# Optimization experiments

Measured on AMD Instinct MI355X. Metric: run time of the kernel, lower is better.

## Reference

```python
import jax, jax.numpy as jnp
import numpy as np

NUM_CLASSES = 26
IGNORE_LABEL = 0
LAMBDA_SMOOTH = 1.0
EPSILON = 1e-05
# static indices of valid (non-ignored) classes
_VALID = np.array([c for c in range(NUM_CLASSES) if c != IGNORE_LABEL])


def setup_inputs() -> dict:
    key = jax.random.key(0)
    k1, k2, k3 = jax.random.split(key, 3)
    B, D, H, W = 1, 160, 192, 224
    fixed_label_map = jax.random.randint(k1, (B, D, H, W), 0, NUM_CLASSES, dtype=jnp.int32)
    warped_moving_label_map = jax.random.randint(k2, (B, D, H, W), 0, NUM_CLASSES, dtype=jnp.int32)
    vector_field = jax.random.normal(k3, (B, 3, D, H, W), dtype=jnp.float32)
    return {
        'fixed_label_map': fixed_label_map,
        'warped_moving_label_map': warped_moving_label_map,
        'vector_field': vector_field,
    }


def _soft_dice(fixed, moving):
    # Equivalent to one-hot expansion + sum over (B,D,H,W), but computed
    # directly from integer labels via histogram counts (single pass).
    f = fixed.reshape(-1)
    m = moving.reshape(-1)
    fixed_vol = jnp.bincount(f, length=NUM_CLASSES).astype(jnp.float32)
    moving_vol = jnp.bincount(m, length=NUM_CLASSES).astype(jnp.float32)
    # intersection[c] = #{voxels: f==c and m==c}
    inter = jnp.bincount(f, weights=(f == m).astype(jnp.float32), length=NUM_CLASSES)
    dice = (2.0 * inter + EPSILON) / (fixed_vol + moving_vol + EPSILON)
    return 1.0 - dice[_VALID].mean()


def _diffusion(vf):
    # vf: [B, 3, D, H, W]
    dz = vf[:, :, 1:, :, :] - vf[:, :, :-1, :, :]
    dy = vf[:, :, :, 1:, :] - vf[:, :, :, :-1, :]
    dx = vf[:, :, :, :, 1:] - vf[:, :, :, :, :-1]
    return (jnp.mean(dz * dz) + jnp.mean(dy * dy) + jnp.mean(dx * dx)) / 3.0


def reference(fixed_label_map, warped_moving_label_map, vector_field):
    similarity_loss = _soft_dice(fixed_label_map, warped_moving_label_map)
    smoothness_loss = _diffusion(vector_field)
    total_loss = similarity_loss + LAMBDA_SMOOTH * smoothness_loss
    return (total_loss, similarity_loss, smoothness_loss)
```

## Files before the change

kernel.cpp:

```cpp
#include <hip/hip_runtime.h>


namespace {
constexpr int NC    = 26;
constexpr int Dd    = 160, Hh = 192, Ww = 224;
constexpr int W4    = Ww / 4;
constexpr int PL4   = Hh * W4;
constexpr int N4L   = Dd * Hh * Ww / 4;
constexpr int JSTRIDE = 33;
constexpr int NBINS   = NC * JSTRIDE;
constexpr int TPB     = 1024;
constexpr int WPB     = TPB / 64;
constexpr int HIST_BLOCKS = 210;
constexpr int HT          = HIST_BLOCKS * TPB;
constexpr int SLAB    = 6;
constexpr int DCH     = 5;
constexpr int DIFF_WAVES  = 3 * (Dd / DCH) * (Hh / SLAB);
constexpr int DIFF_BLOCKS = DIFF_WAVES / WPB;
constexpr int FUSED_BLOCKS = DIFF_BLOCKS + HIST_BLOCKS;
constexpr int GRP         = 8;
constexpr int DIFF_GRPS   = DIFF_BLOCKS / GRP;
constexpr int PAIRED_GRPS = 2 * DIFF_GRPS;
}

__global__ void init_ws_kernel(unsigned int* __restrict__ joint,
                               double* __restrict__ sums) {
    int i = blockIdx.x * blockDim.x + threadIdx.x;
    if (i < NBINS) joint[i] = 0u;
    if (i < 3)     sums[i]  = 0.0;
}

__device__ __forceinline__ void hist_path(
        int hb,
        const int4* __restrict__ f4,
        const int4* __restrict__ m4,
        unsigned int* __restrict__ gj) {
    __shared__ unsigned int h[NBINS];
    for (int i = threadIdx.x; i < NBINS; i += TPB) h[i] = 0u;
    __syncthreads();

    const int g = hb * TPB + threadIdx.x;
    int4 a0 = f4[g];
    int4 a1 = f4[g + HT];
    int4 a2 = f4[g + 2 * HT];
    int4 a3 = f4[g + 3 * HT];
    int4 a4 = f4[g + 4 * HT];
    int4 a5 = f4[g + 5 * HT];
    int4 a6 = f4[g + 6 * HT];
    int4 a7 = f4[g + 7 * HT];
    int4 b0 = m4[g];
    int4 b1 = m4[g + HT];
    int4 b2 = m4[g + 2 * HT];
    int4 b3 = m4[g + 3 * HT];
    int4 b4 = m4[g + 4 * HT];
    int4 b5 = m4[g + 5 * HT];
    int4 b6 = m4[g + 6 * HT];
    int4 b7 = m4[g + 7 * HT];

#define JACC(A, B)                                   \
    atomicAdd(&h[(A).x * JSTRIDE + (B).x], 1u);      \
    atomicAdd(&h[(A).y * JSTRIDE + (B).y], 1u);      \
    atomicAdd(&h[(A).z * JSTRIDE + (B).z], 1u);      \
    atomicAdd(&h[(A).w * JSTRIDE + (B).w], 1u);
    JACC(a0, b0) JACC(a1, b1) JACC(a2, b2) JACC(a3, b3)
    JACC(a4, b4) JACC(a5, b5) JACC(a6, b6) JACC(a7, b7)
#undef JACC

    __syncthreads();
    for (int i = threadIdx.x; i < NBINS; i += TPB) {
        unsigned int v = h[i];
        if (v) atomicAdd(&gj[i], v);
    }
}

__device__ __forceinline__ void diff_path(
        int db,
        const float4* __restrict__ v4,
        double* __restrict__ gs) {
    const int lane = threadIdx.x & 63;
    const int wid  = threadIdx.x >> 6;
    const int w      = db * WPB + wid;
    const int c      = w >> 10;
    const int rem    = w & 1023;
    const int dchunk = rem >> 5;
    const int slab   = rem & 31;
    const int h0     = slab * SLAB;
    const int d0     = dchunk * DCH;
    const bool al    = (lane < W4);
    const bool hv    = (h0 + SLAB < Hh);
    const int  l     = al ? lane : (W4 - 1);

    size_t cur = ((size_t)(c * Dd + d0) * Hh + h0) * W4 + l;

    float4 p0 = v4[cur];
    float4 p1 = v4[cur + W4];
    float4 p2 = v4[cur + 2 * W4];
    float4 p3 = v4[cur + 3 * W4];
    float4 p4 = v4[cur + 4 * W4];
    float4 p5 = v4[cur + 5 * W4];

    float sx = 0.f, sy = 0.f, sz = 0.f;
    const int haloOff = (hv ? SLAB : SLAB - 1) * W4;

    for (int k = 0; k < DCH; ++k) {
        const int d = d0 + k;
        const bool dzv = (d < Dd - 1);
        float4 hl = v4[cur + haloOff];
        float4 n0 = p0, n1 = p1, n2 = p2, n3 = p3, n4 = p4, n5 = p5;
        if (dzv) {
            const size_t nb = cur + PL4;
            n0 = v4[nb];
            n1 = v4[nb + W4];
            n2 = v4[nb + 2 * W4];
            n3 = v4[nb + 3 * W4];
            n4 = v4[nb + 4 * W4];
            n5 = v4[nb + 5 * W4];
        }

#define DX(P)                                                                  \
        {                                                                      \
            float d1 = (P).y - (P).x, d2 = (P).z - (P).y, d3 = (P).w - (P).z;  \
            sx += d1 * d1 + d2 * d2 + d3 * d3;                                 \
            float nx = __shfl_down((P).x, 1);                                  \
            float d4 = nx - (P).w;                                             \
            sx += (lane < W4 - 1) ? d4 * d4 : 0.f;                             \
        }
        DX(p0) DX(p1) DX(p2) DX(p3) DX(p4) DX(p5)
#undef DX
#define DY(A, B)                                                               \
        {                                                                      \
            float e0 = (B).x - (A).x, e1 = (B).y - (A).y;                      \
            float e2 = (B).z - (A).z, e3 = (B).w - (A).w;                      \
            sy += e0 * e0 + e1 * e1 + e2 * e2 + e3 * e3;                       \
        }
        DY(p0, p1) DY(p1, p2) DY(p2, p3) DY(p3, p4) DY(p4, p5)
        if (hv) DY(p5, hl)
#undef DY
        if (dzv) {
#define DZ(A, B)                                                               \
            {                                                                  \
                float e0 = (B).x - (A).x, e1 = (B).y - (A).y;                  \
                float e2 = (B).z - (A).z, e3 = (B).w - (A).w;                  \
                sz += e0 * e0 + e1 * e1 + e2 * e2 + e3 * e3;                   \
            }
            DZ(p0, n0) DZ(p1, n1) DZ(p2, n2) DZ(p3, n3) DZ(p4, n4) DZ(p5, n5)
#undef DZ
        }
        p0 = n0; p1 = n1; p2 = n2; p3 = n3; p4 = n4; p5 = n5;
        cur += PL4;
    }

    if (!al) { sx = 0.f; sy = 0.f; sz = 0.f; }

    #pragma unroll
    for (int off = 32; off > 0; off >>= 1) {
        sx += __shfl_down(sx, off);
        sy += __shfl_down(sy, off);
        sz += __shfl_down(sz, off);
    }
    __shared__ float px[WPB], py[WPB], pz[WPB];
    if (lane == 0) { px[wid] = sx; py[wid] = sy; pz[wid] = sz; }
    __syncthreads();
    if (threadIdx.x == 0) {
        float tx = 0.f, ty = 0.f, tz = 0.f;
        #pragma unroll
        for (int i = 0; i < WPB; ++i) { tx += px[i]; ty += py[i]; tz += pz[i]; }
        atomicAdd(&gs[0], (double)tx);
        atomicAdd(&gs[1], (double)ty);
        atomicAdd(&gs[2], (double)tz);
    }
}

__global__ __launch_bounds__(1024, 4) void fused_kernel(
        const int4* __restrict__ f4,
        const int4* __restrict__ m4,
        unsigned int* __restrict__ gj,
        const float4* __restrict__ v4,
        double* __restrict__ gs) {
    const int grp = blockIdx.x >> 3;
    const int t   = blockIdx.x & 7;
    if (grp < PAIRED_GRPS) {
        const int idx = (grp >> 1) * GRP + t;
        if (grp & 1) hist_path(idx, f4, m4, gj);
        else         diff_path(idx, v4, gs);
    } else {
        hist_path(DIFF_BLOCKS + (blockIdx.x - PAIRED_GRPS * GRP), f4, m4, gj);
    }
}

__global__ void finalize_kernel(const unsigned int* __restrict__ gj,
                                const double* __restrict__ gs,
                                float* __restrict__ out) {
    int lane = threadIdx.x & 63;
    float term = 0.f;
    if (lane >= 1 && lane < NC) {
        float fv = 0.f, mv = 0.f;
        #pragma unroll
        for (int m = 0; m < NC; ++m) fv += (float)gj[lane * JSTRIDE + m];
        #pragma unroll
        for (int f = 0; f < NC; ++f) mv += (float)gj[f * JSTRIDE + lane];
        float iv = (float)gj[lane * JSTRIDE + lane];
        term = (2.f * iv + 1e-5f) / (fv + mv + 1e-5f);
    }
    #pragma unroll
    for (int off = 32; off > 0; off >>= 1) term += __shfl_down(term, off);
    if (threadIdx.x == 0 && blockIdx.x == 0) {
        float sim = 1.f - term * (1.f / 25.f);
        double mdx = gs[0] / ((double)3 * Dd * Hh * (Ww - 1));
        double mdy = gs[1] / ((double)3 * Dd * (Hh - 1) * Ww);
        double mdz = gs[2] / ((double)3 * (Dd - 1) * Hh * Ww);
        float smooth = (float)((mdx + mdy + mdz) / 3.0);
        out[0] = sim + smooth;
        out[1] = sim;
        out[2] = smooth;
    }
}

extern "C" void kernel_launch(void* const* d_in, const int* in_sizes, int n_in,
                              void* d_out, int out_size, void* d_ws, size_t ws_size,
                              hipStream_t stream) {
    const int*   fl = (const int*)d_in[0];
    const int*   ml = (const int*)d_in[1];
    const float* vf = (const float*)d_in[2];
    float* out = (float*)d_out;

    unsigned int* joint = (unsigned int*)d_ws;
    double*       sums  = (double*)((char*)d_ws + 3584);

    init_ws_kernel<<<1, 1024, 0, stream>>>(joint, sums);
    fused_kernel<<<FUSED_BLOCKS, 1024, 0, stream>>>(
        (const int4*)fl, (const int4*)ml, joint, (const float4*)vf, sums);
    finalize_kernel<<<1, 64, 0, stream>>>(joint, sums, out);
}
```

Before: 176.2 us.

## Process two diffusion tiles per wave and halve block size to 512 threads

Each diffusion wave now handles two independent slab tiles (A and B) with interleaved loads, which doubles the memory-level parallelism per wave and halves the number of diffusion waves. Blocks shrink from 1024 to 512 threads, and the histogram block count doubles to keep the same coverage. The interleaved diff/hist block grouping is replaced by all diffusion blocks first, then histogram blocks. Launch bounds change to (512,2), and the larger register footprint per wave may lower occupancy.

```diff
diff --git a/kernel.cpp b/kernel.cpp
--- a/kernel.cpp
+++ b/kernel.cpp
@@ -9,18 +9,16 @@
 constexpr int N4L   = Dd * Hh * Ww / 4;
 constexpr int JSTRIDE = 33;
 constexpr int NBINS   = NC * JSTRIDE;
-constexpr int TPB     = 1024;
+constexpr int TPB     = 512;
 constexpr int WPB     = TPB / 64;
-constexpr int HIST_BLOCKS = 210;
+constexpr int HIST_BLOCKS = 420;
 constexpr int HT          = HIST_BLOCKS * TPB;
 constexpr int SLAB    = 6;
 constexpr int DCH     = 5;
-constexpr int DIFF_WAVES  = 3 * (Dd / DCH) * (Hh / SLAB);
+constexpr int NTILES  = 3 * (Dd / DCH) * (Hh / SLAB);
+constexpr int DIFF_WAVES  = NTILES / 2;
 constexpr int DIFF_BLOCKS = DIFF_WAVES / WPB;
 constexpr int FUSED_BLOCKS = DIFF_BLOCKS + HIST_BLOCKS;
-constexpr int GRP         = 8;
-constexpr int DIFF_GRPS   = DIFF_BLOCKS / GRP;
-constexpr int PAIRED_GRPS = 2 * DIFF_GRPS;
 }
 
 __global__ void init_ws_kernel(unsigned int* __restrict__ joint,
@@ -79,76 +77,109 @@
         double* __restrict__ gs) {
     const int lane = threadIdx.x & 63;
     const int wid  = threadIdx.x >> 6;
-    const int w      = db * WPB + wid;
-    const int c      = w >> 10;
-    const int rem    = w & 1023;
-    const int dchunk = rem >> 5;
-    const int slab   = rem & 31;
-    const int h0     = slab * SLAB;
-    const int d0     = dchunk * DCH;
-    const bool al    = (lane < W4);
-    const bool hv    = (h0 + SLAB < Hh);
-    const int  l     = al ? lane : (W4 - 1);
-
-    size_t cur = ((size_t)(c * Dd + d0) * Hh + h0) * W4 + l;
-
-    float4 p0 = v4[cur];
-    float4 p1 = v4[cur + W4];
-    float4 p2 = v4[cur + 2 * W4];
-    float4 p3 = v4[cur + 3 * W4];
-    float4 p4 = v4[cur + 4 * W4];
-    float4 p5 = v4[cur + 5 * W4];
+    const int w    = db * WPB + wid;
+    const bool al  = (lane < W4);
+    const int  l   = al ? lane : (W4 - 1);
+
+    const int tA = w;
+    const int cA = tA >> 10, remA = tA & 1023;
+    const int d0A = (remA >> 5) * DCH;
+    const int h0A = (remA & 31) * SLAB;
+    const bool hvA = (h0A + SLAB < Hh);
+    const int hOffA = (hvA ? SLAB : SLAB - 1) * W4;
+    size_t curA = ((size_t)(cA * Dd + d0A) * Hh + h0A) * W4 + l;
+    const int tB = w + DIFF_WAVES;
+    const int cB = tB >> 10, remB = tB & 1023;
+    const int d0B = (remB >> 5) * DCH;
+    const int h0B = (remB & 31) * SLAB;
+    const bool hvB = (h0B + SLAB < Hh);
+    const int hOffB = (hvB ? SLAB : SLAB - 1) * W4;
+    size_t curB = ((size_t)(cB * Dd + d0B) * Hh + h0B) * W4 + l;
+
+    float4 pA0 = v4[curA];
+    float4 pA1 = v4[curA + W4];
+    float4 pA2 = v4[curA + 2 * W4];
+    float4 pA3 = v4[curA + 3 * W4];
+    float4 pA4 = v4[curA + 4 * W4];
+    float4 pA5 = v4[curA + 5 * W4];
+    float4 pB0 = v4[curB];
+    float4 pB1 = v4[curB + W4];
+    float4 pB2 = v4[curB + 2 * W4];
+    float4 pB3 = v4[curB + 3 * W4];
+    float4 pB4 = v4[curB + 4 * W4];
+    float4 pB5 = v4[curB + 5 * W4];
 
     float sx = 0.f, sy = 0.f, sz = 0.f;
-    const int haloOff = (hv ? SLAB : SLAB - 1) * W4;
+
+#define DX(P)                                                                  \
+    {                                                                          \
+        float d1 = (P).y - (P).x, d2 = (P).z - (P).y, d3 = (P).w - (P).z;      \
+        sx += d1 * d1 + d2 * d2 + d3 * d3;                                     \
+        float nx = __shfl_down((P).x, 1);                                      \
+        float d4 = nx - (P).w;                                                 \
+        sx += (lane < W4 - 1) ? d4 * d4 : 0.f;                                 \
+    }
+#define DY(A, B)                                                               \
+    {                                                                          \
+        float e0 = (B).x - (A).x, e1 = (B).y - (A).y;                          \
+        float e2 = (B).z - (A).z, e3 = (B).w - (A).w;                          \
+        sy += e0 * e0 + e1 * e1 + e2 * e2 + e3 * e3;                           \
+    }
+#define DZ(A, B)                                                               \
+    {                                                                          \
+        float e0 = (B).x - (A).x, e1 = (B).y - (A).y;                          \
+        float e2 = (B).z - (A).z, e3 = (B).w - (A).w;                          \
+        sz += e0 * e0 + e1 * e1 + e2 * e2 + e3 * e3;                           \
+    }
 
     for (int k = 0; k < DCH; ++k) {
-        const int d = d0 + k;
-        const bool dzv = (d < Dd - 1);
-        float4 hl = v4[cur + haloOff];
-        float4 n0 = p0, n1 = p1, n2 = p2, n3 = p3, n4 = p4, n5 = p5;
-        if (dzv) {
-            const size_t nb = cur + PL4;
-            n0 = v4[nb];
-            n1 = v4[nb + W4];
-            n2 = v4[nb + 2 * W4];
-            n3 = v4[nb + 3 * W4];
-            n4 = v4[nb + 4 * W4];
-            n5 = v4[nb + 5 * W4];
-        }
-
-#define DX(P)                                                                  \
-        {                                                                      \
-            float d1 = (P).y - (P).x, d2 = (P).z - (P).y, d3 = (P).w - (P).z;  \
-            sx += d1 * d1 + d2 * d2 + d3 * d3;                                 \
-            float nx = __shfl_down((P).x, 1);                                  \
-            float d4 = nx - (P).w;                                             \
-            sx += (lane < W4 - 1) ? d4 * d4 : 0.f;                             \
-        }
-        DX(p0) DX(p1) DX(p2) DX(p3) DX(p4) DX(p5)
+        const bool dzvA = (d0A + k < Dd - 1);
+        const bool dzvB = (d0B + k < Dd - 1);
+        float4 hlA = v4[curA + hOffA];
+        float4 hlB = v4[curB + hOffB];
+        float4 nA0 = pA0, nA1 = pA1, nA2 = pA2, nA3 = pA3, nA4 = pA4, nA5 = pA5;
+        if (dzvA) {
+            const size_t nb = curA + PL4;
+            nA0 = v4[nb];
+            nA1 = v4[nb + W4];
+            nA2 = v4[nb + 2 * W4];
+            nA3 = v4[nb + 3 * W4];
+            nA4 = v4[nb + 4 * W4];
+            nA5 = v4[nb + 5 * W4];
+        }
+        float4 nB0 = pB0, nB1 = pB1, nB2 = pB2, nB3 = pB3, nB4 = pB4, nB5 = pB5;
+        if (dzvB) {
+            const size_t nb = curB + PL4;
+            nB0 = v4[nb];
+            nB1 = v4[nb + W4];
+            nB2 = v4[nb + 2 * W4];
+            nB3 = v4[nb + 3 * W4];
+            nB4 = v4[nb + 4 * W4];
+            nB5 = v4[nb + 5 * W4];
+        }
+
+        DX(pA0) DX(pA1) DX(pA2) DX(pA3) DX(pA4) DX(pA5)
+        DY(pA0, pA1) DY(pA1, pA2) DY(pA2, pA3) DY(pA3, pA4) DY(pA4, pA5)
+        if (hvA) DY(pA5, hlA)
+        if (dzvA) {
+            DZ(pA0, nA0) DZ(pA1, nA1) DZ(pA2, nA2)
+            DZ(pA3, nA3) DZ(pA4, nA4) DZ(pA5, nA5)
+        }
+        DX(pB0) DX(pB1) DX(pB2) DX(pB3) DX(pB4) DX(pB5)
+        DY(pB0, pB1) DY(pB1, pB2) DY(pB2, pB3) DY(pB3, pB4) DY(pB4, pB5)
+        if (hvB) DY(pB5, hlB)
+        if (dzvB) {
+            DZ(pB0, nB0) DZ(pB1, nB1) DZ(pB2, nB2)
+            DZ(pB3, nB3) DZ(pB4, nB4) DZ(pB5, nB5)
+        }
+
+        pA0 = nA0; pA1 = nA1; pA2 = nA2; pA3 = nA3; pA4 = nA4; pA5 = nA5;
+        pB0 = nB0; pB1 = nB1; pB2 = nB2; pB3 = nB3; pB4 = nB4; pB5 = nB5;
+        curA += PL4; curB += PL4;
+    }
 #undef DX
-#define DY(A, B)                                                               \
-        {                                                                      \
-            float e0 = (B).x - (A).x, e1 = (B).y - (A).y;                      \
-            float e2 = (B).z - (A).z, e3 = (B).w - (A).w;                      \
-            sy += e0 * e0 + e1 * e1 + e2 * e2 + e3 * e3;                       \
-        }
-        DY(p0, p1) DY(p1, p2) DY(p2, p3) DY(p3, p4) DY(p4, p5)
-        if (hv) DY(p5, hl)
 #undef DY
-        if (dzv) {
-#define DZ(A, B)                                                               \
-            {                                                                  \
-                float e0 = (B).x - (A).x, e1 = (B).y - (A).y;                  \
-                float e2 = (B).z - (A).z, e3 = (B).w - (A).w;                  \
-                sz += e0 * e0 + e1 * e1 + e2 * e2 + e3 * e3;                   \
-            }
-            DZ(p0, n0) DZ(p1, n1) DZ(p2, n2) DZ(p3, n3) DZ(p4, n4) DZ(p5, n5)
 #undef DZ
-        }
-        p0 = n0; p1 = n1; p2 = n2; p3 = n3; p4 = n4; p5 = n5;
-        cur += PL4;
-    }
 
     if (!al) { sx = 0.f; sy = 0.f; sz = 0.f; }
 
@@ -171,21 +202,14 @@
     }
 }
 
-__global__ __launch_bounds__(1024, 4) void fused_kernel(
+__global__ __launch_bounds__(512, 2) void fused_kernel(
         const int4* __restrict__ f4,
         const int4* __restrict__ m4,
         unsigned int* __restrict__ gj,
         const float4* __restrict__ v4,
         double* __restrict__ gs) {
-    const int grp = blockIdx.x >> 3;
-    const int t   = blockIdx.x & 7;
-    if (grp < PAIRED_GRPS) {
-        const int idx = (grp >> 1) * GRP + t;
-        if (grp & 1) hist_path(idx, f4, m4, gj);
-        else         diff_path(idx, v4, gs);
-    } else {
-        hist_path(DIFF_BLOCKS + (blockIdx.x - PAIRED_GRPS * GRP), f4, m4, gj);
-    }
+    if (blockIdx.x < DIFF_BLOCKS) diff_path(blockIdx.x, v4, gs);
+    else                          hist_path(blockIdx.x - DIFF_BLOCKS, f4, m4, gj);
 }
 
 __global__ void finalize_kernel(const unsigned int* __restrict__ gj,
@@ -228,7 +252,7 @@
     double*       sums  = (double*)((char*)d_ws + 3584);
 
     init_ws_kernel<<<1, 1024, 0, stream>>>(joint, sums);
-    fused_kernel<<<FUSED_BLOCKS, 1024, 0, stream>>>(
+    fused_kernel<<<FUSED_BLOCKS, TPB, 0, stream>>>(
         (const int4*)fl, (const int4*)ml, joint, (const float4*)vf, sums);
     finalize_kernel<<<1, 64, 0, stream>>>(joint, sums, out);
 }
```

Result: no change. 174.7 us (median of 3 runs) (-0.9%).
